# Optimization experiments

Measured on AMD Instinct MI355X. Metric: run time of the kernel, lower is better.

## Reference

```python
import jax, jax.numpy as jnp
from jax import lax
import numpy as np

ALPHA = 2.0
EROSIONS = 10


def setup_inputs() -> dict:
    key = jax.random.key(0)
    k1, k2 = jax.random.split(key)
    b, c, h, w = 32, 1, 1024, 1024
    pred = jax.random.uniform(k1, (b, c, h, w), dtype=jnp.float32)
    target = jax.random.randint(k2, (b, c, h, w), 0, 2, dtype=jnp.int32)
    return {"pred": pred, "target": target}


def _perform_erosion(bound, kernel, alpha, erosions):
    # bound: (b, 1, H, W); kernel: (1, 1, 3, 3) cross * 0.2
    def step(carry, k):
        bnd, eroted = carry
        dilation = lax.conv_general_dilated(bnd, kernel, window_strides=(1, 1), padding="SAME")
        erosion = jnp.maximum(dilation - 0.5, 0.0)
        # per-sample global max/min over channel+spatial dims
        emax = jnp.max(erosion, axis=(1, 2, 3), keepdims=True)
        emin = jnp.min(erosion, axis=(1, 2, 3), keepdims=True)
        denom = emax - emin
        safe = jnp.where(denom != 0, denom, jnp.ones_like(denom))
        erosion = jnp.where(denom != 0, (erosion - emin) / safe, erosion)
        eroted = eroted + erosion * (k + 1.0) ** alpha
        return (erosion, eroted), None

    init = (bound, jnp.zeros_like(bound))
    (_, eroted), _ = lax.scan(step, init, jnp.arange(erosions, dtype=bound.dtype))
    return eroted


def reference(pred, target):
    # cross-shaped 3x3 erosion kernel scaled by 0.2 (fixed buffer)
    cross = jnp.array([[0.0, 1.0, 0.0], [1.0, 1.0, 1.0], [0.0, 1.0, 0.0]], dtype=pred.dtype) * 0.2
    kernel = cross[None, None]  # (1, 1, 3, 3)
    c = pred.shape[1]
    losses = []
    for i in range(c):
        tgt = (target == i).astype(pred.dtype)  # (b, c, H, W); c==1 here
        bound = (pred[:, i : i + 1] - tgt) ** 2
        eroted = _perform_erosion(bound, kernel, ALPHA, EROSIONS)
        losses.append(jnp.mean(eroted))
    return jnp.mean(jnp.stack(losses))
```

## Files before the change

kernel.cpp:

```cpp
#include <hip/hip_runtime.h>
#include <hip/hip_fp16.h>
#include <hip/hip_cooperative_groups.h>

namespace cg = cooperative_groups;

#define BATCH 32
#define H 1024
#define W 1024
#define NPIX (H * W)
#define ITERS 10
#define SROWS 16
#define BROWS 32
#define STRIPS (H / BROWS)
#define NBLK (BATCH * STRIPS)

typedef _Float16 half8_t __attribute__((ext_vector_type(8)));

struct Stats {
    unsigned maxbits[ITERS][BATCH];
    unsigned minbits[ITERS][BATCH];
    double   sum[ITERS][BATCH];
};

__global__ void init_stats(Stats* st) {
    int i = blockIdx.x * blockDim.x + threadIdx.x;
    if (i < ITERS * BATCH) {
        (&st->maxbits[0][0])[i] = 0u;
        (&st->minbits[0][0])[i] = 0x7f800000u;
        (&st->sum[0][0])[i]     = 0.0;
    }
}

__device__ __forceinline__ float bound1(const float* __restrict__ pred,
                                        const int* __restrict__ tgt, size_t off) {
    float d = pred[off] - (tgt[off] == 0 ? 1.f : 0.f);
    return d * d;
}

__device__ __forceinline__ void cvt8(half8_t x, float f[8]) {
    #pragma unroll
    for (int j = 0; j < 8; ++j) f[j] = (float)x[j];
}

__device__ __forceinline__ void row_load0(
    const float* __restrict__ pred, const int* __restrict__ target,
    size_t base, int r, int lane128, float f[8], float& L, float& R)
{
    const int  col = lane128 * 8;
    const bool inb = (r >= 0) && (r < H);
    size_t off = base + (size_t)r * W + col;
    if (inb) {
        float4 p0 = *(const float4*)(pred + off);
        float4 p1 = *(const float4*)(pred + off + 4);
        int4   t0 = *(const int4*)(target + off);
        int4   t1 = *(const int4*)(target + off + 4);
        float d;
        d = p0.x - (t0.x == 0 ? 1.f : 0.f); f[0] = d * d;
        d = p0.y - (t0.y == 0 ? 1.f : 0.f); f[1] = d * d;
        d = p0.z - (t0.z == 0 ? 1.f : 0.f); f[2] = d * d;
        d = p0.w - (t0.w == 0 ? 1.f : 0.f); f[3] = d * d;
        d = p1.x - (t1.x == 0 ? 1.f : 0.f); f[4] = d * d;
        d = p1.y - (t1.y == 0 ? 1.f : 0.f); f[5] = d * d;
        d = p1.z - (t1.z == 0 ? 1.f : 0.f); f[6] = d * d;
        d = p1.w - (t1.w == 0 ? 1.f : 0.f); f[7] = d * d;
    } else {
        #pragma unroll
        for (int j = 0; j < 8; ++j) f[j] = 0.f;
    }
    L = __shfl_up(f[7], 1, 64);
    R = __shfl_down(f[0], 1, 64);
    const int wl = lane128 & 63;
    if (!inb) { L = 0.f; R = 0.f; return; }
    if (lane128 == 0)        L = 0.f;
    else if (wl == 0)        L = bound1(pred, target, off - 1);
    if (lane128 == 127)      R = 0.f;
    else if (wl == 63)       R = bound1(pred, target, off + 8);
}

__global__ __launch_bounds__(256, 4) void erode_fused(
    const float* __restrict__ pred, const int* __restrict__ target,
    _Float16* __restrict__ haloTop,
    _Float16* __restrict__ haloBot,
    Stats* __restrict__ st)
{
    cg::grid_group grid = cg::this_grid();
    const int blk = blockIdx.x;
    const int b   = blk >> 5;
    const int s   = blk & (STRIPS - 1);
    const int tid = threadIdx.x;
    const int sub     = tid >> 7;
    const int lane128 = tid & 127;
    const int wv      = tid >> 6;
    const int lane    = tid & 63;
    const int r0  = s * BROWS + sub * SROWS;
    const int col = lane128 * 8;
    const size_t base = (size_t)b * NPIX;

    __shared__ _Float16 eL[4][SROWS];
    __shared__ _Float16 eR[4][SROWS];
    __shared__ half8_t  rowA[128];
    __shared__ half8_t  rowB[128];
    __shared__ float  smax[4];
    __shared__ float  smin[4];
    __shared__ double ssum[4];

    half8_t stor[SROWS];

    {
        float prev[8], cur[8], nxt[8];
        float Lp, Rp, Lc, Rc, Ln, Rn;
        row_load0(pred, target, base, r0 - 1, lane128, prev, Lp, Rp);
        row_load0(pred, target, base, r0,     lane128, cur,  Lc, Rc);

        float  m  = 0.f;
        float  mn = __builtin_inf();
        double sum = 0.0;

        #pragma unroll
        for (int i = 0; i < SROWS; ++i) {
            row_load0(pred, target, base, r0 + i + 1, lane128, nxt, Ln, Rn);
            float e[8];
            #pragma unroll
            for (int j = 0; j < 8; ++j) {
                float lf = (j == 0) ? Lc : cur[j - 1];
                float rf = (j == 7) ? Rc : cur[j + 1];
                float s5 = (cur[j] + lf) + (rf + prev[j]) + nxt[j];
                e[j] = fmaxf(fmaf(s5, 0.2f, -0.5f), 0.f);
            }
            half8_t o;
            #pragma unroll
            for (int j = 0; j < 8; ++j) o[j] = (_Float16)e[j];
            stor[i] = o;

            float rm = fmaxf(fmaxf(fmaxf(e[0], e[1]), fmaxf(e[2], e[3])),
                             fmaxf(fmaxf(e[4], e[5]), fmaxf(e[6], e[7])));
            float rn = fminf(fminf(fminf(e[0], e[1]), fminf(e[2], e[3])),
                             fminf(fminf(e[4], e[5]), fminf(e[6], e[7])));
            float rs = ((e[0] + e[1]) + (e[2] + e[3])) + ((e[4] + e[5]) + (e[6] + e[7]));
            m   = fmaxf(m, rm);
            mn  = fminf(mn, rn);
            sum += (double)rs;
            #pragma unroll
            for (int j = 0; j < 8; ++j) { prev[j] = cur[j]; cur[j] = nxt[j]; }
            Lc = Ln; Rc = Rn;
        }

        #pragma unroll
        for (int off = 32; off > 0; off >>= 1) {
            m   = fmaxf(m,  __shfl_down(m,  off, 64));
            mn  = fminf(mn, __shfl_down(mn, off, 64));
            sum += __shfl_down(sum, off, 64);
        }
        if (lane == 0) { smax[wv] = m; smin[wv] = mn; ssum[wv] = sum; }
        __syncthreads();
        if (tid == 0) {
            m   = fmaxf(fmaxf(smax[0], smax[1]), fmaxf(smax[2], smax[3]));
            mn  = fminf(fminf(smin[0], smin[1]), fminf(smin[2], smin[3]));
            sum = ssum[0] + ssum[1] + ssum[2] + ssum[3];
            atomicMax(&st->maxbits[0][b], __float_as_uint(m));
            atomicMin(&st->minbits[0][b], __float_as_uint(mn));
            atomicAdd(&st->sum[0][b], sum);
        }
        if (sub == 0) *(half8_t*)(haloTop + ((size_t)1 * NBLK + blk) * W + col) = stor[0];
        else          *(half8_t*)(haloBot + ((size_t)1 * NBLK + blk) * W + col) = stor[SROWS - 1];
    }
    grid.sync();

    for (int k = 1; k < ITERS; ++k) {
        const int par = k & 1;

        unsigned mb = __hip_atomic_load(&st->maxbits[k - 1][b], __ATOMIC_RELAXED, __HIP_MEMORY_SCOPE_AGENT);
        unsigned nb = __hip_atomic_load(&st->minbits[k - 1][b], __ATOMIC_RELAXED, __HIP_MEMORY_SCOPE_AGENT);
        float emax = __uint_as_float(mb);
        float emn  = __uint_as_float(nb);
        float denom = emax - emn;
        float sent = 0.f, A = 0.2f, Bc = -0.5f;
        if (denom != 0.f) {
            float invd = 1.f / denom;
            sent = emn;
            A    = 0.2f * invd;
            Bc   = -emn * invd - 0.5f;
        }

        #pragma unroll
        for (int i = 0; i < SROWS; ++i) {
            if (lane == 0)  eL[wv][i] = stor[i][0];
            if (lane == 63) eR[wv][i] = stor[i][7];
        }
        if (sub == 0) rowA[lane128] = stor[SROWS - 1];
        else          rowB[lane128] = stor[0];
        __syncthreads();

        float fprev[8], fcur[8], fnxt[8];
        if (sub == 0) {
            if (s > 0) {
                half8_t h = *(const half8_t*)(haloBot + ((size_t)par * NBLK + blk - 1) * W + col);
                cvt8(h, fprev);
            } else {
                #pragma unroll
                for (int j = 0; j < 8; ++j) fprev[j] = sent;
            }
        } else {
            cvt8(rowA[lane128], fprev);
        }
        cvt8(stor[0], fcur);
        half8_t hdn = {};
        if (sub == 1 && s < STRIPS - 1)
            hdn = *(const half8_t*)(haloTop + ((size_t)par * NBLK + blk + 1) * W + col);

        float  m  = 0.f;
        float  mn = __builtin_inf();
        double sum = 0.0;

        #pragma unroll
        for (int i = 0; i < SROWS; ++i) {
            if (i < SROWS - 1)       cvt8(stor[i + 1], fnxt);
            else if (sub == 0)       cvt8(rowB[lane128], fnxt);
            else if (s < STRIPS - 1) cvt8(hdn, fnxt);
            else {
                #pragma unroll
                for (int j = 0; j < 8; ++j) fnxt[j] = sent;
            }

            float L = __shfl_up(fcur[7], 1, 64);
            float R = __shfl_down(fcur[0], 1, 64);
            if (lane128 == 0)        L = sent;
            else if (lane == 0)      L = (float)eR[wv - 1][i];
            if (lane128 == 127)      R = sent;
            else if (lane == 63)     R = (float)eL[wv + 1][i];

            float e[8];
            #pragma unroll
            for (int j = 0; j < 8; ++j) {
                float lf = (j == 0) ? L : fcur[j - 1];
                float rf = (j == 7) ? R : fcur[j + 1];
                float s5 = (fcur[j] + lf) + (rf + fprev[j]) + fnxt[j];
                e[j] = fmaxf(fmaf(s5, A, Bc), 0.f);
            }

            half8_t o;
            #pragma unroll
            for (int j = 0; j < 8; ++j) o[j] = (_Float16)e[j];
            stor[i] = o;

            float rm = fmaxf(fmaxf(fmaxf(e[0], e[1]), fmaxf(e[2], e[3])),
                             fmaxf(fmaxf(e[4], e[5]), fmaxf(e[6], e[7])));
            float rn = fminf(fminf(fminf(e[0], e[1]), fminf(e[2], e[3])),
                             fminf(fminf(e[4], e[5]), fminf(e[6], e[7])));
            float rs = ((e[0] + e[1]) + (e[2] + e[3])) + ((e[4] + e[5]) + (e[6] + e[7]));
            m   = fmaxf(m, rm);
            mn  = fminf(mn, rn);
            sum += (double)rs;

            #pragma unroll
            for (int j = 0; j < 8; ++j) { fprev[j] = fcur[j]; fcur[j] = fnxt[j]; }
        }

        #pragma unroll
        for (int off = 32; off > 0; off >>= 1) {
            m   = fmaxf(m,  __shfl_down(m,  off, 64));
            mn  = fminf(mn, __shfl_down(mn, off, 64));
            sum += __shfl_down(sum, off, 64);
        }
        if (lane == 0) { smax[wv] = m; smin[wv] = mn; ssum[wv] = sum; }
        __syncthreads();
        if (tid == 0) {
            m   = fmaxf(fmaxf(smax[0], smax[1]), fmaxf(smax[2], smax[3]));
            mn  = fminf(fminf(smin[0], smin[1]), fminf(smin[2], smin[3]));
            sum = ssum[0] + ssum[1] + ssum[2] + ssum[3];
            atomicMax(&st->maxbits[k][b], __float_as_uint(m));
            atomicMin(&st->minbits[k][b], __float_as_uint(mn));
            atomicAdd(&st->sum[k][b], sum);
        }

        if (k < ITERS - 1) {
            const int np = (k + 1) & 1;
            if (sub == 0) *(half8_t*)(haloTop + ((size_t)np * NBLK + blk) * W + col) = stor[0];
            else          *(half8_t*)(haloBot + ((size_t)np * NBLK + blk) * W + col) = stor[SROWS - 1];
            grid.sync();
        }
    }
}

template <int MODE>
__device__ __forceinline__ void row_load8(
    const float* __restrict__ pred, const int* __restrict__ target,
    const _Float16* __restrict__ in, size_t base, int r, int lane128,
    float sent, float f[8], float& L, float& R)
{
    const int  col = lane128 * 8;
    const bool inb = (r >= 0) && (r < H);
    size_t off = base + (size_t)r * W + col;
    if (inb) {
        if (MODE == 0) {
            float4 p0 = *(const float4*)(pred + off);
            float4 p1 = *(const float4*)(pred + off + 4);
            int4   t0 = *(const int4*)(target + off);
            int4   t1 = *(const int4*)(target + off + 4);
            float d;
            d = p0.x - (t0.x == 0 ? 1.f : 0.f); f[0] = d * d;
            d = p0.y - (t0.y == 0 ? 1.f : 0.f); f[1] = d * d;
            d = p0.z - (t0.z == 0 ? 1.f : 0.f); f[2] = d * d;
            d = p0.w - (t0.w == 0 ? 1.f : 0.f); f[3] = d * d;
            d = p1.x - (t1.x == 0 ? 1.f : 0.f); f[4] = d * d;
            d = p1.y - (t1.y == 0 ? 1.f : 0.f); f[5] = d * d;
            d = p1.z - (t1.z == 0 ? 1.f : 0.f); f[6] = d * d;
            d = p1.w - (t1.w == 0 ? 1.f : 0.f); f[7] = d * d;
        } else {
            half8_t x = *(const half8_t*)(in + off);
            #pragma unroll
            for (int j = 0; j < 8; ++j) f[j] = (float)x[j];
        }
    } else {
        #pragma unroll
        for (int j = 0; j < 8; ++j) f[j] = sent;
    }
    L = __shfl_up(f[7], 1, 64);
    R = __shfl_down(f[0], 1, 64);
    const int wl = lane128 & 63;
    if (!inb) { L = sent; R = sent; return; }
    if (lane128 == 0)        L = sent;
    else if (wl == 0)        L = (MODE == 0) ? bound1(pred, target, off - 1) : (float)in[off - 1];
    if (lane128 == 127)      R = sent;
    else if (wl == 63)       R = (MODE == 0) ? bound1(pred, target, off + 8) : (float)in[off + 8];
}

template <int MODE, int STORE>
__global__ __launch_bounds__(256) void erode_strip(
    const float* __restrict__ pred, const int* __restrict__ target,
    const _Float16* __restrict__ in, _Float16* __restrict__ out,
    Stats* __restrict__ st, int iter)
{
    const int blk = blockIdx.x;
    const int b   = blk >> 5;
    const int s   = blk & (STRIPS - 1);
    const int tid = threadIdx.x;
    const int sub     = tid >> 7;
    const int lane128 = tid & 127;
    const int r0  = s * BROWS + sub * SROWS;
    const int col = lane128 * 8;
    const size_t base = (size_t)b * NPIX;

    float sent = 0.f, A = 0.2f, Bc = -0.5f;
    if (MODE == 1) {
        float emax = __uint_as_float(st->maxbits[iter - 1][b]);
        float emn  = __uint_as_float(st->minbits[iter - 1][b]);
        float denom = emax - emn;
        if (denom != 0.f) {
            float invd = 1.f / denom;
            sent = emn;
            A    = 0.2f * invd;
            Bc   = -emn * invd - 0.5f;
        }
    }

    float prev[8], cur[8], nxt[8];
    float Lp, Rp, Lc, Rc, Ln, Rn;
    row_load8<MODE>(pred, target, in, base, r0 - 1, lane128, sent, prev, Lp, Rp);
    row_load8<MODE>(pred, target, in, base, r0,     lane128, sent, cur,  Lc, Rc);

    float  m  = 0.f;
    float  mn = __builtin_inf();
    double sum = 0.0;

    #pragma unroll 2
    for (int i = 0; i < SROWS; ++i) {
        const int r = r0 + i;
        row_load8<MODE>(pred, target, in, base, r + 1, lane128, sent, nxt, Ln, Rn);
        float e[8];
        #pragma unroll
        for (int j = 0; j < 8; ++j) {
            float lf = (j == 0) ? Lc : cur[j - 1];
            float rf = (j == 7) ? Rc : cur[j + 1];
            float s5 = (cur[j] + lf) + (rf + prev[j]) + nxt[j];
            e[j] = fmaxf(fmaf(s5, A, Bc), 0.f);
        }
        if (STORE) {
            half8_t o;
            #pragma unroll
            for (int j = 0; j < 8; ++j) o[j] = (_Float16)e[j];
            *(half8_t*)(out + base + (size_t)r * W + col) = o;
        }
        float rm = fmaxf(fmaxf(fmaxf(e[0], e[1]), fmaxf(e[2], e[3])),
                         fmaxf(fmaxf(e[4], e[5]), fmaxf(e[6], e[7])));
        float rn = fminf(fminf(fminf(e[0], e[1]), fminf(e[2], e[3])),
                         fminf(fminf(e[4], e[5]), fminf(e[6], e[7])));
        float rs = ((e[0] + e[1]) + (e[2] + e[3])) + ((e[4] + e[5]) + (e[6] + e[7]));
        m   = fmaxf(m, rm);
        mn  = fminf(mn, rn);
        sum += (double)rs;
        #pragma unroll
        for (int j = 0; j < 8; ++j) { prev[j] = cur[j]; cur[j] = nxt[j]; }
        Lc = Ln; Rc = Rn;
    }

    #pragma unroll
    for (int off = 32; off > 0; off >>= 1) {
        m   = fmaxf(m,  __shfl_down(m,  off, 64));
        mn  = fminf(mn, __shfl_down(mn, off, 64));
        sum += __shfl_down(sum, off, 64);
    }
    __shared__ float  smax[4];
    __shared__ float  smin[4];
    __shared__ double ssum[4];
    int lane = tid & 63, wave = tid >> 6;
    if (lane == 0) { smax[wave] = m; smin[wave] = mn; ssum[wave] = sum; }
    __syncthreads();
    if (tid == 0) {
        m   = fmaxf(fmaxf(smax[0], smax[1]), fmaxf(smax[2], smax[3]));
        mn  = fminf(fminf(smin[0], smin[1]), fminf(smin[2], smin[3]));
        sum = ssum[0] + ssum[1] + ssum[2] + ssum[3];
        atomicMax(&st->maxbits[iter][b], __float_as_uint(m));
        atomicMin(&st->minbits[iter][b], __float_as_uint(mn));
        atomicAdd(&st->sum[iter][b], sum);
    }
}

__global__ void finalize(const Stats* __restrict__ st, float* __restrict__ out) {
    if (threadIdx.x == 0 && blockIdx.x == 0) {
        double total = 0.0;
        for (int k = 0; k < ITERS; ++k) {
            double w = (double)((k + 1) * (k + 1));
            for (int b = 0; b < BATCH; ++b) {
                float emax  = __uint_as_float(st->maxbits[k][b]);
                float emn   = __uint_as_float(st->minbits[k][b]);
                float denom = emax - emn;
                double s = st->sum[k][b];
                double sn;
                if (denom != 0.f)
                    sn = (s - (double)NPIX * (double)emn) / (double)denom;
                else
                    sn = s;
                total += w * sn;
            }
        }
        out[0] = (float)(total / ((double)BATCH * (double)NPIX));
    }
}

extern "C" void kernel_launch(void* const* d_in, const int* in_sizes, int n_in,
                              void* d_out, int out_size, void* d_ws, size_t ws_size,
                              hipStream_t stream) {
    (void)in_sizes; (void)n_in; (void)out_size;
    const float* pred   = (const float*)d_in[0];
    const int*   target = (const int*)d_in[1];

    const size_t fieldBytes = (size_t)BATCH * NPIX * sizeof(_Float16);
    char* ws = (char*)d_ws;
    _Float16* bufA;
    _Float16* bufB;
    Stats* st;
    if (ws_size >= 2 * fieldBytes + sizeof(Stats)) {
        bufA = (_Float16*)ws;
        bufB = (_Float16*)(ws + fieldBytes);
        st   = (Stats*)(ws + 2 * fieldBytes);
    } else {
        bufA = (_Float16*)ws;
        bufB = (_Float16*)d_in[1];
        st   = (Stats*)(ws + fieldBytes);
    }
    _Float16* haloT = (_Float16*)ws;
    _Float16* haloB = haloT + (size_t)2 * NBLK * W;

    static int mode = -1;
    if (mode < 0) {
        int coop = 0;
        (void)hipDeviceGetAttribute(&coop, hipDeviceAttributeCooperativeLaunch, 0);
        int perCU = 0;
        (void)hipOccupancyMaxActiveBlocksPerMultiprocessor(&perCU, erode_fused, 256, 0);
        int nCU = 0;
        (void)hipDeviceGetAttribute(&nCU, hipDeviceAttributeMultiprocessorCount, 0);
        mode = (coop && perCU > 0 && nCU > 0 && (long)perCU * nCU >= NBLK) ? 1 : 0;
    }

    init_stats<<<1, 320, 0, stream>>>(st);

    bool ran_fused = false;
    if (mode == 1) {
        void* args[5] = { (void*)&pred, (void*)&target, (void*)&haloT, (void*)&haloB, (void*)&st };
        hipError_t e = hipLaunchCooperativeKernel((void*)erode_fused, dim3(NBLK), dim3(256),
                                                  args, 0, stream);
        if (e == hipSuccess) ran_fused = true;
        else mode = 0;
    }

    if (!ran_fused) {
        dim3 grid(NBLK), block(256);
        erode_strip<0, 1><<<grid, block, 0, stream>>>(pred, target, nullptr, bufA, st, 0);
        _Float16* src = bufA;
        _Float16* dst = bufB;
        for (int k = 1; k < ITERS; ++k) {
            if (k == ITERS - 1)
                erode_strip<1, 0><<<grid, block, 0, stream>>>(nullptr, nullptr, src, dst, st, k);
            else
                erode_strip<1, 1><<<grid, block, 0, stream>>>(nullptr, nullptr, src, dst, st, k);
            _Float16* t = src; src = dst; dst = t;
        }
    }

    finalize<<<1, 64, 0, stream>>>(st, (float*)d_out);
}
```

Before: 586.1 us.

## Replace cooperative grid.sync with hierarchical atomic barrier and register-resident rows

Swaps the cooperative-groups grid sync for a custom two-level atomic barrier, with 8 sub-counters feeding one master counter per phase, and launches the fused kernel as a normal launch instead of a cooperative one. It also replaces the indexed half8 array with 16 named registers through macro unrolling, so the rows stay in VGPRs rather than spilling to scratch. The aim is to cut barrier latency, cooperative launch overhead and scratch traffic. The risk is deadlock if not all 1024 blocks are co-resident, since a normal launch does not guarantee residency and only the occupancy check guards it.

Result: no change. 581.7 us (-0.7%).

```diff
diff --git a/kernel.cpp b/kernel.cpp
--- a/kernel.cpp
+++ b/kernel.cpp
@@ -1,8 +1,5 @@
 #include <hip/hip_runtime.h>
 #include <hip/hip_fp16.h>
-#include <hip/hip_cooperative_groups.h>
-
-namespace cg = cooperative_groups;
 
 #define BATCH 32
 #define H 1024
@@ -14,6 +11,10 @@
 #define STRIPS (H / BROWS)
 #define NBLK (BATCH * STRIPS)
 
+#define BAR_STRIDE 16
+#define BAR_SUBWORDS (ITERS * 8 * BAR_STRIDE)
+#define BAR_WORDS    (BAR_SUBWORDS + ITERS * BAR_STRIDE)
+
 typedef _Float16 half8_t __attribute__((ext_vector_type(8)));
 
 struct Stats {
@@ -22,13 +23,14 @@
     double   sum[ITERS][BATCH];
 };
 
-__global__ void init_stats(Stats* st) {
+__global__ void init_all(Stats* st, unsigned* bar) {
     int i = blockIdx.x * blockDim.x + threadIdx.x;
     if (i < ITERS * BATCH) {
         (&st->maxbits[0][0])[i] = 0u;
         (&st->minbits[0][0])[i] = 0x7f800000u;
         (&st->sum[0][0])[i]     = 0.0;
     }
+    for (int j = i; j < BAR_WORDS; j += blockDim.x) bar[j] = 0u;
 }
 
 __device__ __forceinline__ float bound1(const float* __restrict__ pred,
@@ -77,13 +79,91 @@
     else if (wl == 63)       R = bound1(pred, target, off + 8);
 }
 
+__device__ __forceinline__ void gridbar(unsigned* barSub, unsigned* barMst, int phase) {
+    __threadfence();
+    if (threadIdx.x == 0) {
+        unsigned* sc = &barSub[(phase * 8 + (blockIdx.x & 7)) * BAR_STRIDE];
+        unsigned prev = __hip_atomic_fetch_add(sc, 1u, __ATOMIC_ACQ_REL, __HIP_MEMORY_SCOPE_AGENT);
+        if (prev == (NBLK / 8) - 1)
+            __hip_atomic_fetch_add(&barMst[phase * BAR_STRIDE], 1u,
+                                   __ATOMIC_ACQ_REL, __HIP_MEMORY_SCOPE_AGENT);
+        while (__hip_atomic_load(&barMst[phase * BAR_STRIDE],
+                                 __ATOMIC_ACQUIRE, __HIP_MEMORY_SCOPE_AGENT) < 8u)
+            __builtin_amdgcn_s_sleep(2);
+    }
+    __threadfence();
+    __syncthreads();
+}
+
+#define FOR16(X) X(0) X(1) X(2) X(3) X(4) X(5) X(6) X(7) \
+                 X(8) X(9) X(10) X(11) X(12) X(13) X(14) X(15)
+#define FOR15(X) X(0,1) X(1,2) X(2,3) X(3,4) X(4,5) X(5,6) X(6,7) X(7,8) \
+                 X(8,9) X(9,10) X(10,11) X(11,12) X(12,13) X(13,14) X(14,15)
+
+#define ACC_STATS(e)                                                          \
+    { float rm = fmaxf(fmaxf(fmaxf(e[0], e[1]), fmaxf(e[2], e[3])),           \
+                       fmaxf(fmaxf(e[4], e[5]), fmaxf(e[6], e[7])));          \
+      float rn = fminf(fminf(fminf(e[0], e[1]), fminf(e[2], e[3])),           \
+                       fminf(fminf(e[4], e[5]), fminf(e[6], e[7])));          \
+      float rs = ((e[0] + e[1]) + (e[2] + e[3])) + ((e[4] + e[5]) + (e[6] + e[7])); \
+      m = fmaxf(m, rm); mn = fminf(mn, rn); sum += (double)rs; }
+
+#define STEP0(i) {                                                            \
+    row_load0(pred, target, base, r0 + i + 1, lane128, nxt, Ln, Rn);          \
+    float e[8];                                                               \
+    _Pragma("unroll")                                                         \
+    for (int j = 0; j < 8; ++j) {                                             \
+        float lf = (j == 0) ? Lc : cur[j - 1];                                \
+        float rf = (j == 7) ? Rc : cur[j + 1];                                \
+        float s5 = (cur[j] + lf) + (rf + prev[j]) + nxt[j];                   \
+        e[j] = fmaxf(fmaf(s5, 0.2f, -0.5f), 0.f);                             \
+    }                                                                         \
+    half8_t o;                                                                \
+    _Pragma("unroll")                                                         \
+    for (int j = 0; j < 8; ++j) o[j] = (_Float16)e[j];                        \
+    s##i = o;                                                                 \
+    ACC_STATS(e)                                                              \
+    _Pragma("unroll")                                                         \
+    for (int j = 0; j < 8; ++j) { prev[j] = cur[j]; cur[j] = nxt[j]; }        \
+    Lc = Ln; Rc = Rn;                                                         \
+}
+
+#define PUB_EDGE(i) { if (lane == 0)  eL[wv][i] = s##i[0];                    \
+                      if (lane == 63) eR[wv][i] = s##i[7]; }
+
+#define STEP1_CORE(i)                                                         \
+    float L = __shfl_up(fcur[7], 1, 64);                                      \
+    float R = __shfl_down(fcur[0], 1, 64);                                    \
+    if (lane128 == 0)        L = sent;                                        \
+    else if (lane == 0)      L = (float)eR[wv - 1][i];                        \
+    if (lane128 == 127)      R = sent;                                        \
+    else if (lane == 63)     R = (float)eL[wv + 1][i];                        \
+    float e[8];                                                               \
+    _Pragma("unroll")                                                         \
+    for (int j = 0; j < 8; ++j) {                                             \
+        float lf = (j == 0) ? L : fcur[j - 1];                                \
+        float rf = (j == 7) ? R : fcur[j + 1];                                \
+        float s5 = (fcur[j] + lf) + (rf + fprev[j]) + fnxt[j];                \
+        e[j] = fmaxf(fmaf(s5, A, Bc), 0.f);                                   \
+    }                                                                         \
+    half8_t o;                                                                \
+    _Pragma("unroll")                                                         \
+    for (int j = 0; j < 8; ++j) o[j] = (_Float16)e[j];                        \
+    s##i = o;                                                                 \
+    ACC_STATS(e)                                                              \
+    _Pragma("unroll")                                                         \
+    for (int j = 0; j < 8; ++j) { fprev[j] = fcur[j]; fcur[j] = fnxt[j]; }
+
+#define STEP1(i, ip1) { float fnxt[8]; cvt8(s##ip1, fnxt); STEP1_CORE(i) }
+
 __global__ __launch_bounds__(256, 4) void erode_fused(
     const float* __restrict__ pred, const int* __restrict__ target,
     _Float16* __restrict__ haloTop,
     _Float16* __restrict__ haloBot,
-    Stats* __restrict__ st)
+    Stats* __restrict__ st, unsigned* __restrict__ bar)
 {
-    cg::grid_group grid = cg::this_grid();
+    unsigned* barSub = bar;
+    unsigned* barMst = bar + BAR_SUBWORDS;
     const int blk = blockIdx.x;
     const int b   = blk >> 5;
     const int s   = blk & (STRIPS - 1);
@@ -104,7 +184,8 @@
     __shared__ float  smin[4];
     __shared__ double ssum[4];
 
-    half8_t stor[SROWS];
+    half8_t s0, s1, s2, s3, s4, s5r, s6, s7, s8, s9, s10, s11, s12, s13, s14, s15;
+    #define s5 s5r
 
     {
         float prev[8], cur[8], nxt[8];
@@ -116,34 +197,7 @@
         float  mn = __builtin_inf();
         double sum = 0.0;
 
-        #pragma unroll
-        for (int i = 0; i < SROWS; ++i) {
-            row_load0(pred, target, base, r0 + i + 1, lane128, nxt, Ln, Rn);
-            float e[8];
-            #pragma unroll
-            for (int j = 0; j < 8; ++j) {
-                float lf = (j == 0) ? Lc : cur[j - 1];
-                float rf = (j == 7) ? Rc : cur[j + 1];
-                float s5 = (cur[j] + lf) + (rf + prev[j]) + nxt[j];
-                e[j] = fmaxf(fmaf(s5, 0.2f, -0.5f), 0.f);
-            }
-            half8_t o;
-            #pragma unroll
-            for (int j = 0; j < 8; ++j) o[j] = (_Float16)e[j];
-            stor[i] = o;
-
-            float rm = fmaxf(fmaxf(fmaxf(e[0], e[1]), fmaxf(e[2], e[3])),
-                             fmaxf(fmaxf(e[4], e[5]), fmaxf(e[6], e[7])));
-            float rn = fminf(fminf(fminf(e[0], e[1]), fminf(e[2], e[3])),
-                             fminf(fminf(e[4], e[5]), fminf(e[6], e[7])));
-            float rs = ((e[0] + e[1]) + (e[2] + e[3])) + ((e[4] + e[5]) + (e[6] + e[7]));
-            m   = fmaxf(m, rm);
-            mn  = fminf(mn, rn);
-            sum += (double)rs;
-            #pragma unroll
-            for (int j = 0; j < 8; ++j) { prev[j] = cur[j]; cur[j] = nxt[j]; }
-            Lc = Ln; Rc = Rn;
-        }
+        FOR16(STEP0)
 
         #pragma unroll
         for (int off = 32; off > 0; off >>= 1) {
@@ -161,16 +215,16 @@
             atomicMin(&st->minbits[0][b], __float_as_uint(mn));
             atomicAdd(&st->sum[0][b], sum);
         }
-        if (sub == 0) *(half8_t*)(haloTop + ((size_t)1 * NBLK + blk) * W + col) = stor[0];
-        else          *(half8_t*)(haloBot + ((size_t)1 * NBLK + blk) * W + col) = stor[SROWS - 1];
-    }
-    grid.sync();
+        if (sub == 0) *(half8_t*)(haloTop + ((size_t)1 * NBLK + blk) * W + col) = s0;
+        else          *(half8_t*)(haloBot + ((size_t)1 * NBLK + blk) * W + col) = s15;
+    }
+    gridbar(barSub, barMst, 0);
 
     for (int k = 1; k < ITERS; ++k) {
         const int par = k & 1;
 
-        unsigned mb = __hip_atomic_load(&st->maxbits[k - 1][b], __ATOMIC_RELAXED, __HIP_MEMORY_SCOPE_AGENT);
-        unsigned nb = __hip_atomic_load(&st->minbits[k - 1][b], __ATOMIC_RELAXED, __HIP_MEMORY_SCOPE_AGENT);
+        unsigned mb = __hip_atomic_load(&st->maxbits[k - 1][b], __ATOMIC_ACQUIRE, __HIP_MEMORY_SCOPE_AGENT);
+        unsigned nb = __hip_atomic_load(&st->minbits[k - 1][b], __ATOMIC_ACQUIRE, __HIP_MEMORY_SCOPE_AGENT);
         float emax = __uint_as_float(mb);
         float emn  = __uint_as_float(nb);
         float denom = emax - emn;
@@ -182,16 +236,12 @@
             Bc   = -emn * invd - 0.5f;
         }
 
-        #pragma unroll
-        for (int i = 0; i < SROWS; ++i) {
-            if (lane == 0)  eL[wv][i] = stor[i][0];
-            if (lane == 63) eR[wv][i] = stor[i][7];
-        }
-        if (sub == 0) rowA[lane128] = stor[SROWS - 1];
-        else          rowB[lane128] = stor[0];
+        FOR16(PUB_EDGE)
+        if (sub == 0) rowA[lane128] = s15;
+        else          rowB[lane128] = s0;
         __syncthreads();
 
-        float fprev[8], fcur[8], fnxt[8];
+        float fprev[8], fcur[8];
         if (sub == 0) {
             if (s > 0) {
                 half8_t h = *(const half8_t*)(haloBot + ((size_t)par * NBLK + blk - 1) * W + col);
@@ -203,7 +253,7 @@
         } else {
             cvt8(rowA[lane128], fprev);
         }
-        cvt8(stor[0], fcur);
+        cvt8(s0, fcur);
         half8_t hdn = {};
         if (sub == 1 && s < STRIPS - 1)
             hdn = *(const half8_t*)(haloTop + ((size_t)par * NBLK + blk + 1) * W + col);
@@ -212,48 +262,16 @@
         float  mn = __builtin_inf();
         double sum = 0.0;
 
-        #pragma unroll
-        for (int i = 0; i < SROWS; ++i) {
-            if (i < SROWS - 1)       cvt8(stor[i + 1], fnxt);
-            else if (sub == 0)       cvt8(rowB[lane128], fnxt);
+        FOR15(STEP1)
+        {
+            float fnxt[8];
+            if (sub == 0)            cvt8(rowB[lane128], fnxt);
             else if (s < STRIPS - 1) cvt8(hdn, fnxt);
             else {
                 #pragma unroll
                 for (int j = 0; j < 8; ++j) fnxt[j] = sent;
             }
-
-            float L = __shfl_up(fcur[7], 1, 64);
-            float R = __shfl_down(fcur[0], 1, 64);
-            if (lane128 == 0)        L = sent;
-            else if (lane == 0)      L = (float)eR[wv - 1][i];
-            if (lane128 == 127)      R = sent;
-            else if (lane == 63)     R = (float)eL[wv + 1][i];
-
-            float e[8];
-            #pragma unroll
-            for (int j = 0; j < 8; ++j) {
-                float lf = (j == 0) ? L : fcur[j - 1];
-                float rf = (j == 7) ? R : fcur[j + 1];
-                float s5 = (fcur[j] + lf) + (rf + fprev[j]) + fnxt[j];
-                e[j] = fmaxf(fmaf(s5, A, Bc), 0.f);
-            }
-
-            half8_t o;
-            #pragma unroll
-            for (int j = 0; j < 8; ++j) o[j] = (_Float16)e[j];
-            stor[i] = o;
-
-            float rm = fmaxf(fmaxf(fmaxf(e[0], e[1]), fmaxf(e[2], e[3])),
-                             fmaxf(fmaxf(e[4], e[5]), fmaxf(e[6], e[7])));
-            float rn = fminf(fminf(fminf(e[0], e[1]), fminf(e[2], e[3])),
-                             fminf(fminf(e[4], e[5]), fminf(e[6], e[7])));
-            float rs = ((e[0] + e[1]) + (e[2] + e[3])) + ((e[4] + e[5]) + (e[6] + e[7]));
-            m   = fmaxf(m, rm);
-            mn  = fminf(mn, rn);
-            sum += (double)rs;
-
-            #pragma unroll
-            for (int j = 0; j < 8; ++j) { fprev[j] = fcur[j]; fcur[j] = fnxt[j]; }
+            STEP1_CORE(15)
         }
 
         #pragma unroll
@@ -275,11 +293,12 @@
 
         if (k < ITERS - 1) {
             const int np = (k + 1) & 1;
-            if (sub == 0) *(half8_t*)(haloTop + ((size_t)np * NBLK + blk) * W + col) = stor[0];
-            else          *(half8_t*)(haloBot + ((size_t)np * NBLK + blk) * W + col) = stor[SROWS - 1];
-            grid.sync();
-        }
-    }
+            if (sub == 0) *(half8_t*)(haloTop + ((size_t)np * NBLK + blk) * W + col) = s0;
+            else          *(half8_t*)(haloBot + ((size_t)np * NBLK + blk) * W + col) = s15;
+            gridbar(barSub, barMst, k);
+        }
+    }
+    #undef s5
 }
 
 template <int MODE>
@@ -381,14 +400,7 @@
             for (int j = 0; j < 8; ++j) o[j] = (_Float16)e[j];
             *(half8_t*)(out + base + (size_t)r * W + col) = o;
         }
-        float rm = fmaxf(fmaxf(fmaxf(e[0], e[1]), fmaxf(e[2], e[3])),
-                         fmaxf(fmaxf(e[4], e[5]), fmaxf(e[6], e[7])));
-        float rn = fminf(fminf(fminf(e[0], e[1]), fminf(e[2], e[3])),
-                         fminf(fminf(e[4], e[5]), fminf(e[6], e[7])));
-        float rs = ((e[0] + e[1]) + (e[2] + e[3])) + ((e[4] + e[5]) + (e[6] + e[7]));
-        m   = fmaxf(m, rm);
-        mn  = fminf(mn, rn);
-        sum += (double)rs;
+        ACC_STATS(e)
         #pragma unroll
         for (int j = 0; j < 8; ++j) { prev[j] = cur[j]; cur[j] = nxt[j]; }
         Lc = Ln; Rc = Rn;
@@ -461,30 +473,22 @@
     }
     _Float16* haloT = (_Float16*)ws;
     _Float16* haloB = haloT + (size_t)2 * NBLK * W;
+    unsigned* bar   = (unsigned*)(haloB + (size_t)2 * NBLK * W);
 
     static int mode = -1;
     if (mode < 0) {
-        int coop = 0;
-        (void)hipDeviceGetAttribute(&coop, hipDeviceAttributeCooperativeLaunch, 0);
         int perCU = 0;
         (void)hipOccupancyMaxActiveBlocksPerMultiprocessor(&perCU, erode_fused, 256, 0);
         int nCU = 0;
         (void)hipDeviceGetAttribute(&nCU, hipDeviceAttributeMultiprocessorCount, 0);
-        mode = (coop && perCU > 0 && nCU > 0 && (long)perCU * nCU >= NBLK) ? 1 : 0;
-    }
-
-    init_stats<<<1, 320, 0, stream>>>(st);
-
-    bool ran_fused = false;
+        mode = (perCU > 0 && nCU > 0 && (long)perCU * nCU >= NBLK) ? 1 : 0;
+    }
+
+    init_all<<<1, 512, 0, stream>>>(st, bar);
+
     if (mode == 1) {
-        void* args[5] = { (void*)&pred, (void*)&target, (void*)&haloT, (void*)&haloB, (void*)&st };
-        hipError_t e = hipLaunchCooperativeKernel((void*)erode_fused, dim3(NBLK), dim3(256),
-                                                  args, 0, stream);
-        if (e == hipSuccess) ran_fused = true;
-        else mode = 0;
-    }
-
-    if (!ran_fused) {
+        erode_fused<<<dim3(NBLK), dim3(256), 0, stream>>>(pred, target, haloT, haloB, st, bar);
+    } else {
         dim3 grid(NBLK), block(256);
         erode_strip<0, 1><<<grid, block, 0, stream>>>(pred, target, nullptr, bufA, st, 0);
         _Float16* src = bufA;
```
